# Performance work log

Hardware: AMD Instinct MI355X
Metric: run time of the kernel (lower is better)

The kernel has to match this reference:

```python
import jax, jax.numpy as jnp
import numpy as np

N_NODES = 8192
K = 64


def setup_inputs() -> dict:
    key = jax.random.key(0)
    k1, k2 = jax.random.split(key)
    A = jax.random.normal(k1, (N_NODES, N_NODES), dtype=jnp.float32)
    idx = jax.random.randint(k2, (N_NODES,), 0, N_NODES, dtype=jnp.int64)
    return {"A": A, "idx": idx}


def reference(A, idx):
    # adj = relu(A)
    adj = jax.nn.relu(A)
    # per-row top-k indices (dim=1), then scatter a 0/1 mask and multiply
    _, ind = jax.lax.top_k(adj, K)  # ind: [N, K]
    rows = jnp.arange(adj.shape[0], dtype=ind.dtype)[:, None]  # [N, 1]
    mask = jnp.zeros_like(adj).at[rows, ind].set(1.0)
    return adj * mask
```

## Files before the change

### kernel.cpp

```cpp
#include <hip/hip_runtime.h>
#include <stdint.h>


typedef float f32x4 __attribute__((ext_vector_type(4)));

constexpr int N      = 8192;
constexpr int K      = 64;
constexpr int BLOCK  = 256;
constexpr int VPT    = N / BLOCK;
constexpr int V4     = VPT / 4;
constexpr int CAP    = 1536;
constexpr int EQ_CAP = 256;

__device__ __forceinline__ uint32_t wave_reduce_add(uint32_t x) {
    #pragma unroll
    for (int d = 32; d >= 1; d >>= 1) x += __shfl_down(x, d, 64);
    return x;
}

__device__ __forceinline__ void scan_pick2(const uint32_t (*h)[256],
                                           uint32_t* s_prefix, uint32_t* s_k,
                                           uint32_t* s_hb, int shift, int lane) {
    uint32_t k  = *s_k;
    uint32_t h0 = h[0][4*lane+0] + h[1][4*lane+0] + h[2][4*lane+0] + h[3][4*lane+0];
    uint32_t h1 = h[0][4*lane+1] + h[1][4*lane+1] + h[2][4*lane+1] + h[3][4*lane+1];
    uint32_t h2 = h[0][4*lane+2] + h[1][4*lane+2] + h[2][4*lane+2] + h[3][4*lane+2];
    uint32_t h3 = h[0][4*lane+3] + h[1][4*lane+3] + h[2][4*lane+3] + h[3][4*lane+3];
    uint32_t suf = h0 + h1 + h2 + h3;
    #pragma unroll
    for (int d = 1; d < 64; d <<= 1) {
        uint32_t o = __shfl_down(suf, d, 64);
        if (lane + d < 64) suf += o;
    }
    unsigned long long m = __ballot(suf >= k);
    int cl = 63 - __builtin_clzll(m);
    if (lane == cl) {
        uint32_t S0 = suf, S1 = S0 - h0, S2 = S1 - h1, S3 = S2 - h2;
        int b; uint32_t Sb, hb;
        if      (S3 >= k) { b = 3; Sb = S3; hb = h3; }
        else if (S2 >= k) { b = 2; Sb = S2; hb = h2; }
        else if (S1 >= k) { b = 1; Sb = S1; hb = h1; }
        else              { b = 0; Sb = S0; hb = h0; }
        *s_prefix |= (uint32_t)(4*lane + b) << shift;
        *s_k  = k - (Sb - hb);
        *s_hb = hb;
    }
}

__global__ __launch_bounds__(BLOCK) void topk_row_kernel(
    const float* __restrict__ A, float* __restrict__ out)
{
    __shared__ uint32_t hist[2][4][256];
    __shared__ uint32_t list[CAP];
    __shared__ uint32_t s_eq[EQ_CAP];
    __shared__ uint32_t s_rb[4][3];
    __shared__ uint32_t s_rmax[4];
    __shared__ uint32_t s_prefix, s_k, s_hb, s_T, s_cnt, s_listcnt, s_min;

    const int tid  = threadIdx.x;
    const int wave = tid >> 6;
    const int lane = tid & 63;
    const int row  = blockIdx.x;

    const float4* rowp = reinterpret_cast<const float4*>(A + (size_t)row * N);
    float4*       outp = reinterpret_cast<float4*>(out + (size_t)row * N);

    uint32_t v[VPT];
    uint32_t mx = 0;
    #pragma unroll
    for (int j = 0; j < V4; ++j) {
        float4 f = rowp[tid + j * BLOCK];
        uint32_t x0 = (f.x > 0.f) ? __float_as_uint(f.x) : 0u;
        uint32_t x1 = (f.y > 0.f) ? __float_as_uint(f.y) : 0u;
        uint32_t x2 = (f.z > 0.f) ? __float_as_uint(f.z) : 0u;
        uint32_t x3 = (f.w > 0.f) ? __float_as_uint(f.w) : 0u;
        v[4*j+0] = x0; v[4*j+1] = x1; v[4*j+2] = x2; v[4*j+3] = x3;
        uint32_t m01 = x0 > x1 ? x0 : x1;
        uint32_t m23 = x2 > x3 ? x2 : x3;
        uint32_t mm  = m01 > m23 ? m01 : m23;
        mx = mm > mx ? mm : mx;
    }
    #pragma unroll
    for (int d = 32; d >= 1; d >>= 1) {
        uint32_t o = __shfl_down(mx, d, 64);
        mx = o > mx ? o : mx;
    }
    if (lane == 0) s_rmax[wave] = mx;
    if (tid == 0) { s_listcnt = 0; s_cnt = 0; }
    __syncthreads();
    uint32_t ma = s_rmax[0], mb = s_rmax[1], mc = s_rmax[2], md = s_rmax[3];
    ma = mb > ma ? mb : ma; mc = md > mc ? md : mc;
    const uint32_t expM = (mc > ma ? mc : ma) >> 23;

    uint32_t cm0 = 0, cm1 = 0, cm2 = 0, cm3 = 0, mnz = 0;
    #pragma unroll
    for (int j = 0; j < VPT; ++j) {
        uint32_t x = v[j];
        if (x != 0u) {
            uint32_t d   = expM - (x >> 23);
            uint32_t bit = 1u << j;
            mnz |= bit;
            if      (d == 0u) cm0 |= bit;
            else if (d == 1u) cm1 |= bit;
            else if (d == 2u) cm2 |= bit;
            else if (d == 3u) cm3 |= bit;
        }
    }
    uint32_t r01 = (uint32_t)__popc(cm0) | ((uint32_t)__popc(cm1) << 16);
    uint32_t r23 = (uint32_t)__popc(cm2) | ((uint32_t)__popc(cm3) << 16);
    uint32_t rcp = (uint32_t)__popc(mnz);
    r01 = wave_reduce_add(r01);
    r23 = wave_reduce_add(r23);
    rcp = wave_reduce_add(rcp);
    if (lane == 0) { s_rb[wave][0] = r01; s_rb[wave][1] = r23; s_rb[wave][2] = rcp; }
    __syncthreads();
    uint32_t t01  = s_rb[0][0] + s_rb[1][0] + s_rb[2][0] + s_rb[3][0];
    uint32_t t23  = s_rb[0][1] + s_rb[1][1] + s_rb[2][1] + s_rb[3][1];
    uint32_t cpos = s_rb[0][2] + s_rb[1][2] + s_rb[2][2] + s_rb[3][2];
    uint32_t B0 = t01 & 0xFFFFu, B1 = t01 >> 16;
    uint32_t B2 = t23 & 0xFFFFu, B3 = t23 >> 16;

    if (cpos < (uint32_t)K) {
        #pragma unroll
        for (int j = 0; j < V4; ++j) {
            float4 o;
            o.x = __uint_as_float(v[4*j+0]); o.y = __uint_as_float(v[4*j+1]);
            o.z = __uint_as_float(v[4*j+2]); o.w = __uint_as_float(v[4*j+3]);
            __builtin_nontemporal_store(*(const f32x4*)&o,
                                        (f32x4*)&outp[tid + j * BLOCK]);
        }
        return;
    }

    uint32_t cum1 = B0 + B1, cum2 = cum1 + B2, cum3 = cum2 + B3;
    const bool windowOK = (cum3 >= (uint32_t)K);
    uint32_t C, kk, hbInit, prefixInit, ecut, sel = 0;
    bool needExp;
    if (windowOK) {
        uint32_t jf, cumBefore;
        if      (B0   >= (uint32_t)K) { jf = 0; cumBefore = 0;    C = B0; sel = cm0; }
        else if (cum1 >= (uint32_t)K) { jf = 1; cumBefore = B0;   C = B1; sel = cm1; }
        else if (cum2 >= (uint32_t)K) { jf = 2; cumBefore = cum1; C = B2; sel = cm2; }
        else                          { jf = 3; cumBefore = cum2; C = B3; sel = cm3; }
        ecut       = expM - jf;
        kk         = (uint32_t)K - cumBefore;
        hbInit     = C;
        prefixInit = ecut << 23;
        needExp    = false;
    } else {
        ecut = (expM > 7u) ? (expM - 7u) : 0u;
        for (;;) {
            uint32_t lc = 0;
            #pragma unroll
            for (int j = 0; j < VPT; ++j) {
                uint32_t x = v[j];
                lc += (x != 0u && (x >> 23) >= ecut) ? 1u : 0u;
            }
            lc = wave_reduce_add(lc);
            __syncthreads();
            if (lane == 0) s_rb[wave][0] = lc;
            __syncthreads();
            C = s_rb[0][0] + s_rb[1][0] + s_rb[2][0] + s_rb[3][0];
            if (C >= (uint32_t)K || ecut == 0u) break;
            ecut = (ecut > 4u) ? (ecut - 4u) : 0u;
        }
        kk = (uint32_t)K; hbInit = 0xFFFFFFFFu; prefixInit = 0u;
        needExp = true;
    }
    if (tid == 0) { s_prefix = prefixInit; s_k = kk; s_hb = hbInit; }

    int resShift = 23;
    uint32_t T = 0, need = 1;
    auto radix = [&](auto&& forEach, bool needE) {
        int buf = 0;
        if (needE) {
            forEach([&](uint32_t x) { atomicAdd(&hist[0][wave][x >> 23], 1u); });
            __syncthreads();
            if (wave == 0) scan_pick2(hist[0], &s_prefix, &s_k, &s_hb, 23, lane);
            __syncthreads();
            buf = 1;
        }
        for (int shift = 16; shift >= 0; shift -= 8) {
            if (s_hb == 1u) break;
            const uint32_t prefix = s_prefix;
            const uint32_t himask = ~0u << resShift;
            #pragma unroll
            for (int b = lane; b < 256; b += 64) hist[buf ^ 1][wave][b] = 0;
            forEach([&](uint32_t x) {
                if ((x & himask) == prefix)
                    atomicAdd(&hist[buf][wave][(x >> shift) & 255u], 1u);
            });
            __syncthreads();
            if (wave == 0) scan_pick2(hist[buf], &s_prefix, &s_k, &s_hb, shift, lane);
            __syncthreads();
            buf ^= 1;
            resShift = shift;
        }
        if (s_hb == 1u && resShift > 0) {
            const uint32_t mlo = ~0u << resShift;
            const uint32_t pfx = s_prefix;
            forEach([&](uint32_t x) { if ((x & mlo) == pfx) s_T = x; });
            __syncthreads();
            T = s_T;
        } else {
            T = s_prefix;
        }
        need = s_k;
    };

    if (C <= (uint32_t)CAP) {
        uint32_t lsel;
        if (windowOK) {
            lsel = sel;
        } else {
            lsel = 0;
            #pragma unroll
            for (int j = 0; j < VPT; ++j) {
                uint32_t x = v[j];
                if (x != 0u && (x >> 23) >= ecut) lsel |= 1u << j;
            }
        }
        uint32_t lc   = (uint32_t)__popc(lsel);
        uint32_t incl = lc;
        #pragma unroll
        for (int d = 1; d < 64; d <<= 1) {
            uint32_t t = __shfl_up(incl, d, 64);
            if (lane >= d) incl += t;
        }
        uint32_t baseV = 0;
        if (lane == 63) baseV = atomicAdd(&s_listcnt, incl);
        uint32_t base = __shfl(baseV, 63, 64);
        uint32_t pos  = base + (incl - lc);
        #pragma unroll
        for (int j = 0; j < VPT; ++j)
            if (lsel & (1u << j)) list[pos++] = v[j];
        #pragma unroll
        for (int b = lane; b < 256; b += 64) { hist[0][wave][b] = 0; hist[1][wave][b] = 0; }
        __syncthreads();

        auto forEachList = [&](auto&& f) {
            for (uint32_t i = tid; i < C; i += BLOCK) f(list[i]);
        };
        radix(forEachList, needExp);
    } else {
        #pragma unroll
        for (int b = lane; b < 256; b += 64) { hist[0][wave][b] = 0; hist[1][wave][b] = 0; }
        __syncthreads();

        auto forEachReg = [&](auto&& f) {
            #pragma unroll
            for (int j = 0; j < VPT; ++j) if (v[j] != 0u) f(v[j]);
        };
        radix(forEachReg, needExp);
    }

    const float Tf = __uint_as_float(T);
    #pragma unroll
    for (int j = 0; j < V4; ++j) {
        const int base = (tid + j * BLOCK) * 4;
        float4 o;
        float* oc = &o.x;
        #pragma unroll
        for (int c = 0; c < 4; ++c) {
            uint32_t x = v[4*j+c];
            float val = 0.f;
            if (x > T) {
                val = __uint_as_float(x);
            } else if (x == T) {
                uint32_t p = atomicAdd(&s_cnt, 1u);
                if (p < (uint32_t)EQ_CAP) s_eq[p] = (uint32_t)(base + c);
            }
            oc[c] = val;
        }
        __builtin_nontemporal_store(*(const f32x4*)&o,
                                    (f32x4*)&outp[tid + j * BLOCK]);
    }
    __syncthreads();

    const uint32_t cnt = s_cnt;
    if (cnt <= (uint32_t)EQ_CAP) {
        if (tid == 0) {
            for (uint32_t n = 0; n < need; ++n) {
                uint32_t best = 0xFFFFFFFFu, bi = 0;
                for (uint32_t i = 0; i < cnt; ++i)
                    if (s_eq[i] < best) { best = s_eq[i]; bi = i; }
                if (best != 0xFFFFFFFFu) {
                    s_eq[bi] = 0xFFFFFFFFu;
                    out[(size_t)row * N + best] = Tf;
                }
            }
        }
    } else {
        uint32_t last = 0;
        for (uint32_t n = 0; n < need; ++n) {
            __syncthreads();
            if (tid == 0) s_min = 0xFFFFFFFFu;
            __syncthreads();
            #pragma unroll
            for (int j = 0; j < VPT; ++j) {
                if (v[j] == T) {
                    uint32_t g = (uint32_t)(tid + (j >> 2) * BLOCK) * 4u
                               + (uint32_t)(j & 3);
                    if (n == 0 || g > last) atomicMin(&s_min, g);
                }
            }
            __syncthreads();
            last = s_min;
            if (tid == 0 && last != 0xFFFFFFFFu) out[(size_t)row * N + last] = Tf;
        }
    }
}

extern "C" void kernel_launch(void* const* d_in, const int* in_sizes, int n_in,
                              void* d_out, int out_size, void* d_ws, size_t ws_size,
                              hipStream_t stream) {
    const float* A = (const float*)d_in[0];
    float* out = (float*)d_out;
    topk_row_kernel<<<N, BLOCK, 0, stream>>>(A, out);
}
```

Measured before the change: 458.6 us.

## Process one row per wavefront with wave-local radix select, removing block barriers

Each row now goes to a single 64-lane wavefront, and each block handles four rows. All reductions become wave shuffles, and the histogram and candidate list are wave-private in LDS, so no __syncthreads are needed. Each thread holds 128 values in registers, which raises register pressure; launch bounds request 2 blocks per CU. Fallback paths re-read the row from global memory instead of keeping a register copy. Ties are resolved by rescanning global memory. Stores are no longer nontemporal.

New measurement: 456.4 us. No clear change (-0.5%).

```diff
diff --git a/kernel.cpp b/kernel.cpp
--- a/kernel.cpp
+++ b/kernel.cpp
@@ -2,311 +2,262 @@
 #include <stdint.h>
 
 
-typedef float f32x4 __attribute__((ext_vector_type(4)));
-
-constexpr int N      = 8192;
-constexpr int K      = 64;
-constexpr int BLOCK  = 256;
-constexpr int VPT    = N / BLOCK;
-constexpr int V4     = VPT / 4;
-constexpr int CAP    = 1536;
-constexpr int EQ_CAP = 256;
-
-__device__ __forceinline__ uint32_t wave_reduce_add(uint32_t x) {
-    #pragma unroll
-    for (int d = 32; d >= 1; d >>= 1) x += __shfl_down(x, d, 64);
+constexpr int N     = 8192;
+constexpr int K     = 64;
+constexpr int BLOCK = 256;
+constexpr int RPB   = 4;
+constexpr int VPT   = N / 64;
+constexpr int V4    = VPT / 4;
+constexpr int CAP   = 1536;
+
+__device__ __forceinline__ uint32_t bf_max(uint32_t x) {
+    #pragma unroll
+    for (int d = 32; d >= 1; d >>= 1) {
+        uint32_t o = (uint32_t)__shfl_xor((int)x, d, 64);
+        x = o > x ? o : x;
+    }
     return x;
 }
-
-__device__ __forceinline__ void scan_pick2(const uint32_t (*h)[256],
-                                           uint32_t* s_prefix, uint32_t* s_k,
-                                           uint32_t* s_hb, int shift, int lane) {
-    uint32_t k  = *s_k;
-    uint32_t h0 = h[0][4*lane+0] + h[1][4*lane+0] + h[2][4*lane+0] + h[3][4*lane+0];
-    uint32_t h1 = h[0][4*lane+1] + h[1][4*lane+1] + h[2][4*lane+1] + h[3][4*lane+1];
-    uint32_t h2 = h[0][4*lane+2] + h[1][4*lane+2] + h[2][4*lane+2] + h[3][4*lane+2];
-    uint32_t h3 = h[0][4*lane+3] + h[1][4*lane+3] + h[2][4*lane+3] + h[3][4*lane+3];
+__device__ __forceinline__ uint32_t bf_add(uint32_t x) {
+    #pragma unroll
+    for (int d = 32; d >= 1; d >>= 1) x += (uint32_t)__shfl_xor((int)x, d, 64);
+    return x;
+}
+__device__ __forceinline__ uint32_t bf_min(uint32_t x) {
+    #pragma unroll
+    for (int d = 32; d >= 1; d >>= 1) {
+        uint32_t o = (uint32_t)__shfl_xor((int)x, d, 64);
+        x = o < x ? o : x;
+    }
+    return x;
+}
+
+__device__ __forceinline__ void pick_digit(const uint32_t* __restrict__ h,
+                                           int lane, int shift,
+                                           uint32_t& prefix, uint32_t& k,
+                                           uint32_t& hb) {
+    uint4 hv = *reinterpret_cast<const uint4*>(&h[4 * lane]);
+    uint32_t h0 = hv.x, h1 = hv.y, h2 = hv.z, h3 = hv.w;
     uint32_t suf = h0 + h1 + h2 + h3;
     #pragma unroll
     for (int d = 1; d < 64; d <<= 1) {
-        uint32_t o = __shfl_down(suf, d, 64);
-        if (lane + d < 64) suf += o;
+        uint32_t o = (uint32_t)__shfl_down((int)suf, d, 64);
+        suf += (lane + d < 64) ? o : 0u;
     }
     unsigned long long m = __ballot(suf >= k);
     int cl = 63 - __builtin_clzll(m);
-    if (lane == cl) {
-        uint32_t S0 = suf, S1 = S0 - h0, S2 = S1 - h1, S3 = S2 - h2;
-        int b; uint32_t Sb, hb;
-        if      (S3 >= k) { b = 3; Sb = S3; hb = h3; }
-        else if (S2 >= k) { b = 2; Sb = S2; hb = h2; }
-        else if (S1 >= k) { b = 1; Sb = S1; hb = h1; }
-        else              { b = 0; Sb = S0; hb = h0; }
-        *s_prefix |= (uint32_t)(4*lane + b) << shift;
-        *s_k  = k - (Sb - hb);
-        *s_hb = hb;
-    }
-}
-
-__global__ __launch_bounds__(BLOCK) void topk_row_kernel(
+    uint32_t S0 = suf, S1 = S0 - h0, S2 = S1 - h1, S3 = S2 - h2;
+    int b; uint32_t Sb, hbl;
+    if      (S3 >= k) { b = 3; Sb = S3; hbl = h3; }
+    else if (S2 >= k) { b = 2; Sb = S2; hbl = h2; }
+    else if (S1 >= k) { b = 1; Sb = S1; hbl = h1; }
+    else              { b = 0; Sb = S0; hbl = h0; }
+    uint32_t dig  = (uint32_t)(4 * lane + b);
+    uint32_t knew = k - (Sb - hbl);
+    dig  = (uint32_t)__shfl((int)dig,  cl, 64);
+    knew = (uint32_t)__shfl((int)knew, cl, 64);
+    hb   = (uint32_t)__shfl((int)hbl,  cl, 64);
+    prefix |= dig << shift;
+    k = knew;
+}
+
+__global__ __launch_bounds__(BLOCK, 2) void topk_row_kernel(
     const float* __restrict__ A, float* __restrict__ out)
 {
-    __shared__ uint32_t hist[2][4][256];
-    __shared__ uint32_t list[CAP];
-    __shared__ uint32_t s_eq[EQ_CAP];
-    __shared__ uint32_t s_rb[4][3];
-    __shared__ uint32_t s_rmax[4];
-    __shared__ uint32_t s_prefix, s_k, s_hb, s_T, s_cnt, s_listcnt, s_min;
+    __shared__ __align__(16) uint32_t lds_list[RPB][CAP];
+    __shared__ __align__(16) uint32_t lds_hist[RPB][2][256];
 
     const int tid  = threadIdx.x;
-    const int wave = tid >> 6;
+    const int wv   = tid >> 6;
     const int lane = tid & 63;
-    const int row  = blockIdx.x;
-
-    const float4* rowp = reinterpret_cast<const float4*>(A + (size_t)row * N);
-    float4*       outp = reinterpret_cast<float4*>(out + (size_t)row * N);
+    const int row  = blockIdx.x * RPB + wv;
+
+    uint32_t (&list)[CAP]    = lds_list[wv];
+    uint32_t (&hist)[2][256] = lds_hist[wv];
+
+    const float*  rp  = A + (size_t)row * N;
+    const float4* rp4 = reinterpret_cast<const float4*>(rp);
+    float4*       op4 = reinterpret_cast<float4*>(out + (size_t)row * N);
 
     uint32_t v[VPT];
     uint32_t mx = 0;
     #pragma unroll
-    for (int j = 0; j < V4; ++j) {
-        float4 f = rowp[tid + j * BLOCK];
+    for (int i = 0; i < V4; ++i) {
+        float4 f = rp4[lane + i * 64];
         uint32_t x0 = (f.x > 0.f) ? __float_as_uint(f.x) : 0u;
         uint32_t x1 = (f.y > 0.f) ? __float_as_uint(f.y) : 0u;
         uint32_t x2 = (f.z > 0.f) ? __float_as_uint(f.z) : 0u;
         uint32_t x3 = (f.w > 0.f) ? __float_as_uint(f.w) : 0u;
-        v[4*j+0] = x0; v[4*j+1] = x1; v[4*j+2] = x2; v[4*j+3] = x3;
-        uint32_t m01 = x0 > x1 ? x0 : x1;
-        uint32_t m23 = x2 > x3 ? x2 : x3;
-        uint32_t mm  = m01 > m23 ? m01 : m23;
-        mx = mm > mx ? mm : mx;
-    }
-    #pragma unroll
-    for (int d = 32; d >= 1; d >>= 1) {
-        uint32_t o = __shfl_down(mx, d, 64);
-        mx = o > mx ? o : mx;
-    }
-    if (lane == 0) s_rmax[wave] = mx;
-    if (tid == 0) { s_listcnt = 0; s_cnt = 0; }
-    __syncthreads();
-    uint32_t ma = s_rmax[0], mb = s_rmax[1], mc = s_rmax[2], md = s_rmax[3];
-    ma = mb > ma ? mb : ma; mc = md > mc ? md : mc;
-    const uint32_t expM = (mc > ma ? mc : ma) >> 23;
-
-    uint32_t cm0 = 0, cm1 = 0, cm2 = 0, cm3 = 0, mnz = 0;
+        v[4*i+0] = x0; v[4*i+1] = x1; v[4*i+2] = x2; v[4*i+3] = x3;
+        uint32_t a = x0 > x1 ? x0 : x1;
+        uint32_t b = x2 > x3 ? x2 : x3;
+        uint32_t c = a > b ? a : b;
+        mx = c > mx ? c : mx;
+    }
+    mx = bf_max(mx);
+    const uint32_t expM = mx >> 23;
+
+    uint32_t b0 = 0, b1 = 0, b2 = 0, b3 = 0, cp = 0;
     #pragma unroll
     for (int j = 0; j < VPT; ++j) {
         uint32_t x = v[j];
         if (x != 0u) {
-            uint32_t d   = expM - (x >> 23);
-            uint32_t bit = 1u << j;
-            mnz |= bit;
-            if      (d == 0u) cm0 |= bit;
-            else if (d == 1u) cm1 |= bit;
-            else if (d == 2u) cm2 |= bit;
-            else if (d == 3u) cm3 |= bit;
-        }
-    }
-    uint32_t r01 = (uint32_t)__popc(cm0) | ((uint32_t)__popc(cm1) << 16);
-    uint32_t r23 = (uint32_t)__popc(cm2) | ((uint32_t)__popc(cm3) << 16);
-    uint32_t rcp = (uint32_t)__popc(mnz);
-    r01 = wave_reduce_add(r01);
-    r23 = wave_reduce_add(r23);
-    rcp = wave_reduce_add(rcp);
-    if (lane == 0) { s_rb[wave][0] = r01; s_rb[wave][1] = r23; s_rb[wave][2] = rcp; }
-    __syncthreads();
-    uint32_t t01  = s_rb[0][0] + s_rb[1][0] + s_rb[2][0] + s_rb[3][0];
-    uint32_t t23  = s_rb[0][1] + s_rb[1][1] + s_rb[2][1] + s_rb[3][1];
-    uint32_t cpos = s_rb[0][2] + s_rb[1][2] + s_rb[2][2] + s_rb[3][2];
-    uint32_t B0 = t01 & 0xFFFFu, B1 = t01 >> 16;
-    uint32_t B2 = t23 & 0xFFFFu, B3 = t23 >> 16;
-
-    if (cpos < (uint32_t)K) {
-        #pragma unroll
-        for (int j = 0; j < V4; ++j) {
-            float4 o;
-            o.x = __uint_as_float(v[4*j+0]); o.y = __uint_as_float(v[4*j+1]);
-            o.z = __uint_as_float(v[4*j+2]); o.w = __uint_as_float(v[4*j+3]);
-            __builtin_nontemporal_store(*(const f32x4*)&o,
-                                        (f32x4*)&outp[tid + j * BLOCK]);
-        }
-        return;
-    }
-
-    uint32_t cum1 = B0 + B1, cum2 = cum1 + B2, cum3 = cum2 + B3;
-    const bool windowOK = (cum3 >= (uint32_t)K);
-    uint32_t C, kk, hbInit, prefixInit, ecut, sel = 0;
-    bool needExp;
-    if (windowOK) {
-        uint32_t jf, cumBefore;
-        if      (B0   >= (uint32_t)K) { jf = 0; cumBefore = 0;    C = B0; sel = cm0; }
-        else if (cum1 >= (uint32_t)K) { jf = 1; cumBefore = B0;   C = B1; sel = cm1; }
-        else if (cum2 >= (uint32_t)K) { jf = 2; cumBefore = cum1; C = B2; sel = cm2; }
-        else                          { jf = 3; cumBefore = cum2; C = B3; sel = cm3; }
-        ecut       = expM - jf;
-        kk         = (uint32_t)K - cumBefore;
-        hbInit     = C;
-        prefixInit = ecut << 23;
-        needExp    = false;
-    } else {
-        ecut = (expM > 7u) ? (expM - 7u) : 0u;
-        for (;;) {
-            uint32_t lc = 0;
+            uint32_t d = expM - (x >> 23);
+            cp += 1u;
+            b0 += (d == 0u); b1 += (d == 1u); b2 += (d == 2u); b3 += (d == 3u);
+        }
+    }
+    uint32_t r01  = bf_add(b0 | (b1 << 16));
+    uint32_t r23  = bf_add(b2 | (b3 << 16));
+    uint32_t cpos = bf_add(cp);
+    uint32_t B0 = r01 & 0xFFFFu, B1 = r01 >> 16;
+    uint32_t B2 = r23 & 0xFFFFu, B3 = r23 >> 16;
+
+    uint32_t T = 1u;
+    bool keepAll = true;
+    uint32_t needOut = 0;
+
+    if (cpos >= (uint32_t)K) {
+        uint32_t cum1 = B0 + B1, cum2 = cum1 + B2, cum3 = cum2 + B3;
+        const bool windowOK = (cum3 >= (uint32_t)K);
+
+        uint32_t prefix, k, hb, elow, ehigh, C, lc = 0;
+        int resShift;
+        bool needExp;
+        if (windowOK) {
+            uint32_t cumBefore;
+            uint32_t jf;
+            if      (B0   >= (uint32_t)K) { jf = 0; cumBefore = 0;    C = B0; lc = b0; }
+            else if (cum1 >= (uint32_t)K) { jf = 1; cumBefore = B0;   C = B1; lc = b1; }
+            else if (cum2 >= (uint32_t)K) { jf = 2; cumBefore = cum1; C = B2; lc = b2; }
+            else                          { jf = 3; cumBefore = cum2; C = B3; lc = b3; }
+            uint32_t ecut = expM - jf;
+            k        = (uint32_t)K - cumBefore;
+            hb       = C;
+            prefix   = ecut << 23;
+            resShift = 23;
+            needExp  = false;
+            elow = ehigh = ecut;
+        } else {
+            k = (uint32_t)K; hb = cpos; prefix = 0u; resShift = 32;
+            needExp = true; elow = 0u; ehigh = 255u; C = 0xFFFFFFFFu;
+        }
+
+        auto radix = [&](auto&& forEach) {
+            int buf = 0;
+            for (int s = needExp ? 23 : 16; s >= 0; s = (s == 23) ? 16 : (s - 8)) {
+                if (hb == 1u || hb == k) break;
+                uint4 z; z.x = 0u; z.y = 0u; z.z = 0u; z.w = 0u;
+                *reinterpret_cast<uint4*>(&hist[buf][4 * lane]) = z;
+                __asm__ volatile("" ::: "memory");
+                const uint32_t himask = (resShift >= 32) ? 0u : (~0u << resShift);
+                const uint32_t pfx = prefix;
+                forEach([&](uint32_t x) {
+                    if ((x & himask) == pfx)
+                        atomicAdd(&hist[buf][(x >> s) & 255u], 1u);
+                });
+                __asm__ volatile("" ::: "memory");
+                pick_digit(hist[buf], lane, s, prefix, k, hb);
+                resShift = (s == 23) ? 23 : s;
+                buf ^= 1;
+            }
+            if (hb == 1u && resShift > 0) {
+                const uint32_t himask = (resShift >= 32) ? 0u : (~0u << resShift);
+                const uint32_t pfx = prefix;
+                uint32_t fx = 0u, fnd = 0u;
+                forEach([&](uint32_t x) {
+                    if ((x & himask) == pfx) { fx = x; fnd = 1u; }
+                });
+                unsigned long long m = __ballot(fnd != 0u);
+                int src = __builtin_ctzll(m);
+                T = (uint32_t)__shfl((int)fx, src, 64);
+                keepAll = true;
+            } else if (hb == k && resShift > 0) {
+                const uint32_t himask = (resShift >= 32) ? 0u : (~0u << resShift);
+                const uint32_t pfx = prefix;
+                uint32_t mn = 0xFFFFFFFFu;
+                forEach([&](uint32_t x) {
+                    if ((x & himask) == pfx) mn = x < mn ? x : mn;
+                });
+                T = bf_min(mn);
+                keepAll = true;
+            } else {
+                T = prefix;
+                keepAll = (k == hb);
+                needOut = k;
+            }
+        };
+
+        if (windowOK && C <= (uint32_t)CAP) {
+            uint32_t incl = lc;
+            #pragma unroll
+            for (int d = 1; d < 64; d <<= 1) {
+                uint32_t t = (uint32_t)__shfl_up((int)incl, d, 64);
+                if (lane >= d) incl += t;
+            }
+            uint32_t pos = incl - lc;
+            const uint32_t ecut = elow;
             #pragma unroll
             for (int j = 0; j < VPT; ++j) {
                 uint32_t x = v[j];
-                lc += (x != 0u && (x >> 23) >= ecut) ? 1u : 0u;
-            }
-            lc = wave_reduce_add(lc);
-            __syncthreads();
-            if (lane == 0) s_rb[wave][0] = lc;
-            __syncthreads();
-            C = s_rb[0][0] + s_rb[1][0] + s_rb[2][0] + s_rb[3][0];
-            if (C >= (uint32_t)K || ecut == 0u) break;
-            ecut = (ecut > 4u) ? (ecut - 4u) : 0u;
-        }
-        kk = (uint32_t)K; hbInit = 0xFFFFFFFFu; prefixInit = 0u;
-        needExp = true;
-    }
-    if (tid == 0) { s_prefix = prefixInit; s_k = kk; s_hb = hbInit; }
-
-    int resShift = 23;
-    uint32_t T = 0, need = 1;
-    auto radix = [&](auto&& forEach, bool needE) {
-        int buf = 0;
-        if (needE) {
-            forEach([&](uint32_t x) { atomicAdd(&hist[0][wave][x >> 23], 1u); });
-            __syncthreads();
-            if (wave == 0) scan_pick2(hist[0], &s_prefix, &s_k, &s_hb, 23, lane);
-            __syncthreads();
-            buf = 1;
-        }
-        for (int shift = 16; shift >= 0; shift -= 8) {
-            if (s_hb == 1u) break;
-            const uint32_t prefix = s_prefix;
-            const uint32_t himask = ~0u << resShift;
-            #pragma unroll
-            for (int b = lane; b < 256; b += 64) hist[buf ^ 1][wave][b] = 0;
-            forEach([&](uint32_t x) {
-                if ((x & himask) == prefix)
-                    atomicAdd(&hist[buf][wave][(x >> shift) & 255u], 1u);
+                if (x != 0u && (x >> 23) == ecut) list[pos++] = x;
+            }
+            __asm__ volatile("" ::: "memory");
+            const uint32_t Cc = C;
+            radix([&](auto&& f) {
+                for (uint32_t i = (uint32_t)lane; i < Cc; i += 64u) f(list[i]);
             });
-            __syncthreads();
-            if (wave == 0) scan_pick2(hist[buf], &s_prefix, &s_k, &s_hb, shift, lane);
-            __syncthreads();
-            buf ^= 1;
-            resShift = shift;
-        }
-        if (s_hb == 1u && resShift > 0) {
-            const uint32_t mlo = ~0u << resShift;
-            const uint32_t pfx = s_prefix;
-            forEach([&](uint32_t x) { if ((x & mlo) == pfx) s_T = x; });
-            __syncthreads();
-            T = s_T;
         } else {
-            T = s_prefix;
-        }
-        need = s_k;
-    };
-
-    if (C <= (uint32_t)CAP) {
-        uint32_t lsel;
-        if (windowOK) {
-            lsel = sel;
-        } else {
-            lsel = 0;
-            #pragma unroll
-            for (int j = 0; j < VPT; ++j) {
-                uint32_t x = v[j];
-                if (x != 0u && (x >> 23) >= ecut) lsel |= 1u << j;
-            }
-        }
-        uint32_t lc   = (uint32_t)__popc(lsel);
-        uint32_t incl = lc;
+            const uint32_t el = elow, eh = ehigh;
+            radix([&](auto&& f) {
+                for (int i = lane; i < N; i += 64) {
+                    float fv = rp[i];
+                    uint32_t x = (fv > 0.f) ? __float_as_uint(fv) : 0u;
+                    if (x != 0u) {
+                        uint32_t e = x >> 23;
+                        if (e >= el && e <= eh) f(x);
+                    }
+                }
+            });
+        }
+    }
+
+    if (keepAll) {
         #pragma unroll
-        for (int d = 1; d < 64; d <<= 1) {
-            uint32_t t = __shfl_up(incl, d, 64);
-            if (lane >= d) incl += t;
-        }
-        uint32_t baseV = 0;
-        if (lane == 63) baseV = atomicAdd(&s_listcnt, incl);
-        uint32_t base = __shfl(baseV, 63, 64);
-        uint32_t pos  = base + (incl - lc);
-        #pragma unroll
-        for (int j = 0; j < VPT; ++j)
-            if (lsel & (1u << j)) list[pos++] = v[j];
-        #pragma unroll
-        for (int b = lane; b < 256; b += 64) { hist[0][wave][b] = 0; hist[1][wave][b] = 0; }
-        __syncthreads();
-
-        auto forEachList = [&](auto&& f) {
-            for (uint32_t i = tid; i < C; i += BLOCK) f(list[i]);
-        };
-        radix(forEachList, needExp);
+        for (int i = 0; i < V4; ++i) {
+            float4 o;
+            o.x = (v[4*i+0] >= T) ? __uint_as_float(v[4*i+0]) : 0.f;
+            o.y = (v[4*i+1] >= T) ? __uint_as_float(v[4*i+1]) : 0.f;
+            o.z = (v[4*i+2] >= T) ? __uint_as_float(v[4*i+2]) : 0.f;
+            o.w = (v[4*i+3] >= T) ? __uint_as_float(v[4*i+3]) : 0.f;
+            op4[lane + i * 64] = o;
+        }
     } else {
         #pragma unroll
-        for (int b = lane; b < 256; b += 64) { hist[0][wave][b] = 0; hist[1][wave][b] = 0; }
-        __syncthreads();
-
-        auto forEachReg = [&](auto&& f) {
-            #pragma unroll
-            for (int j = 0; j < VPT; ++j) if (v[j] != 0u) f(v[j]);
-        };
-        radix(forEachReg, needExp);
-    }
-
-    const float Tf = __uint_as_float(T);
-    #pragma unroll
-    for (int j = 0; j < V4; ++j) {
-        const int base = (tid + j * BLOCK) * 4;
-        float4 o;
-        float* oc = &o.x;
-        #pragma unroll
-        for (int c = 0; c < 4; ++c) {
-            uint32_t x = v[4*j+c];
-            float val = 0.f;
-            if (x > T) {
-                val = __uint_as_float(x);
-            } else if (x == T) {
-                uint32_t p = atomicAdd(&s_cnt, 1u);
-                if (p < (uint32_t)EQ_CAP) s_eq[p] = (uint32_t)(base + c);
-            }
-            oc[c] = val;
-        }
-        __builtin_nontemporal_store(*(const f32x4*)&o,
-                                    (f32x4*)&outp[tid + j * BLOCK]);
-    }
-    __syncthreads();
-
-    const uint32_t cnt = s_cnt;
-    if (cnt <= (uint32_t)EQ_CAP) {
-        if (tid == 0) {
-            for (uint32_t n = 0; n < need; ++n) {
-                uint32_t best = 0xFFFFFFFFu, bi = 0;
-                for (uint32_t i = 0; i < cnt; ++i)
-                    if (s_eq[i] < best) { best = s_eq[i]; bi = i; }
-                if (best != 0xFFFFFFFFu) {
-                    s_eq[bi] = 0xFFFFFFFFu;
-                    out[(size_t)row * N + best] = Tf;
+        for (int i = 0; i < V4; ++i) {
+            float4 o;
+            o.x = (v[4*i+0] > T) ? __uint_as_float(v[4*i+0]) : 0.f;
+            o.y = (v[4*i+1] > T) ? __uint_as_float(v[4*i+1]) : 0.f;
+            o.z = (v[4*i+2] > T) ? __uint_as_float(v[4*i+2]) : 0.f;
+            o.w = (v[4*i+3] > T) ? __uint_as_float(v[4*i+3]) : 0.f;
+            op4[lane + i * 64] = o;
+        }
+        __asm__ volatile("s_waitcnt vmcnt(0)" ::: "memory");
+        const float Tf = __uint_as_float(T);
+        uint32_t last = 0u; bool first = true;
+        for (uint32_t n = 0; n < needOut; ++n) {
+            uint32_t mylow = 0xFFFFFFFFu;
+            for (int i = lane; i < N; i += 64) {
+                float fv = rp[i];
+                if (fv > 0.f && __float_as_uint(fv) == T) {
+                    uint32_t col = (uint32_t)i;
+                    if ((first || col > last) && col < mylow) mylow = col;
                 }
             }
-        }
-    } else {
-        uint32_t last = 0;
-        for (uint32_t n = 0; n < need; ++n) {
-            __syncthreads();
-            if (tid == 0) s_min = 0xFFFFFFFFu;
-            __syncthreads();
-            #pragma unroll
-            for (int j = 0; j < VPT; ++j) {
-                if (v[j] == T) {
-                    uint32_t g = (uint32_t)(tid + (j >> 2) * BLOCK) * 4u
-                               + (uint32_t)(j & 3);
-                    if (n == 0 || g > last) atomicMin(&s_min, g);
-                }
-            }
-            __syncthreads();
-            last = s_min;
-            if (tid == 0 && last != 0xFFFFFFFFu) out[(size_t)row * N + last] = Tf;
+            uint32_t w = bf_min(mylow);
+            if (w == 0xFFFFFFFFu) break;
+            if (lane == 0) out[(size_t)row * N + w] = Tf;
+            last = w; first = false;
         }
     }
 }
@@ -316,5 +267,5 @@
                               hipStream_t stream) {
     const float* A = (const float*)d_in[0];
     float* out = (float*)d_out;
-    topk_row_kernel<<<N, BLOCK, 0, stream>>>(A, out);
-}
+    topk_row_kernel<<<N / RPB, BLOCK, 0, stream>>>(A, out);
+}
```
